# Kernel optimization log

Measured on AMD Instinct MI355X. Metric: run time of the kernel, lower is better.

Reference implementation:

```python
import jax, jax.numpy as jnp
import numpy as np
import math

B, S, H, K = 512, 200, 256, 16

def setup_inputs() -> dict:
    key = jax.random.key(0)
    ks = jax.random.split(key, 8)
    scale = 1.0 / math.sqrt(H)
    return {
        "input_tensor": jax.random.normal(ks[0], (B, S, H), dtype=jnp.float32),
        "item_mask": jax.random.randint(ks[1], (B, S, 1), 0, 2) > 0,
        "time_f_w_matrix": jax.random.uniform(ks[2], (B, S, 1), dtype=jnp.float32),
        "W1": jax.random.normal(ks[3], (H, H), dtype=jnp.float32) * scale,
        "b1": jnp.zeros((H,), dtype=jnp.float32),
        "W2": jax.random.normal(ks[4], (H, H), dtype=jnp.float32) * scale,
        "b2": jnp.zeros((H,), dtype=jnp.float32),
        "W3": jax.random.normal(ks[5], (H, K), dtype=jnp.float32) * scale,
    }

def reference(input_tensor, item_mask, time_f_w_matrix, W1, b1, W2, b2, W3):
    # small MLP: two Linear+ReLU then bias-free Linear to k_interests
    h = jax.nn.relu(jnp.einsum('bsh,hd->bsd', input_tensor, W1) + b1)
    h = jax.nn.relu(jnp.einsum('bsh,hd->bsd', h, W2) + b2)
    D = jnp.einsum('bsh,hk->bsk', h, W3)              # [B,S,K]
    D = jax.nn.softmax(D, axis=-1)                    # softmax over interests
    mask = item_mask[:, :, 0:1]                       # [B,S,1] bool, broadcast over K
    D = jnp.where(mask, D, jnp.float32(-10000.0))
    D = D / jnp.float32(math.sqrt(K))
    D = jax.nn.softmax(D, axis=-2)                    # softmax over sequence
    D = time_f_w_matrix[:, :, 0:1] * D                # time weighting
    # einsum 'nij,nik->nkj': pool items into K interest vectors
    return jnp.einsum('bsh,bsk->bkh', input_tensor, D)
```

## Files before the change

kernel.cpp:

```cpp
#include <hip/hip_runtime.h>
#include <math.h>

#define HDIM 256
#define KDIM 16
#define SDIM 200
#define BDIM 512
#define NROWS (BDIM * SDIM)
#define TM 32

typedef __bf16 bf16x8 __attribute__((ext_vector_type(8)));
typedef __bf16 bf16x4 __attribute__((ext_vector_type(4)));
typedef float  f32x4  __attribute__((ext_vector_type(4)));

__global__ __launch_bounds__(256) void pack_all(
    const float* __restrict__ W1, const float* __restrict__ W2,
    const float* __restrict__ W3,
    __bf16* __restrict__ w1h, __bf16* __restrict__ w1l,
    __bf16* __restrict__ w2h, __bf16* __restrict__ w2l,
    __bf16* __restrict__ w3h, __bf16* __restrict__ w3l)
{
    int gid = blockIdx.x * 256 + threadIdx.x;
    const float* src;
    __bf16 *oh, *ol;
    int e, N;
    if (gid < 65536)       { src = W1; oh = w1h; ol = w1l; e = gid;          N = 256; }
    else if (gid < 131072) { src = W2; oh = w2h; ol = w2l; e = gid - 65536;  N = 256; }
    else if (gid < 135168) { src = W3; oh = w3h; ol = w3l; e = gid - 131072; N = 16;  }
    else return;

    int j  = e & 7;
    int n  = (e >> 3) & (N - 1);
    int kg = e >> 3; kg = (N == 256) ? (kg >> 8) : (kg >> 4);
    int k  = kg * 8 + j;
    float v = src[k * N + n];
    __bf16 h = (__bf16)v;
    oh[e] = h;
    ol[e] = (__bf16)(v - (float)h);
}

__global__ __launch_bounds__(256) void mlp_softk_mfma(
    const float* __restrict__ X, const int* __restrict__ mask,
    const __bf16* __restrict__ W1h, const __bf16* __restrict__ W1l,
    const float* __restrict__ b1,
    const __bf16* __restrict__ W2h, const __bf16* __restrict__ W2l,
    const float* __restrict__ b2,
    const __bf16* __restrict__ W3h, const __bf16* __restrict__ W3l,
    float* __restrict__ P)
{
    __shared__ __bf16 Ahi[TM * HDIM];
    __shared__ __bf16 Alo[TM * HDIM];

    const int tid  = threadIdx.x;
    const int lane = tid & 63;
    const int w    = tid >> 6;
    const int l15  = lane & 15;
    const int quad = lane >> 4;
    const long r0  = (long)blockIdx.x * TM;

    {
        const float4* Xt = (const float4*)(X + r0 * HDIM);
        #pragma unroll
        for (int t = 0; t < (TM * HDIM / 4) / 256; ++t) {
            int v4  = tid + t * 256;
            float4 f = Xt[v4];
            int row = v4 >> 6;
            int col = (v4 & 63) << 2;
            int kgs = (col >> 3) ^ (row & 31);
            int base = row * HDIM + kgs * 8 + (col & 7);
            __bf16 h0 = (__bf16)f.x, h1 = (__bf16)f.y,
                   h2 = (__bf16)f.z, h3 = (__bf16)f.w;
            bf16x4 hv = {h0, h1, h2, h3};
            bf16x4 lv = {(__bf16)(f.x - (float)h0), (__bf16)(f.y - (float)h1),
                         (__bf16)(f.z - (float)h2), (__bf16)(f.w - (float)h3)};
            *(bf16x4*)(&Ahi[base]) = hv;
            *(bf16x4*)(&Alo[base]) = lv;
        }
    }
    __syncthreads();

    f32x4 acc[2][4];

    auto layer = [&](const __bf16* __restrict__ Wh, const __bf16* __restrict__ Wl,
                     const float* __restrict__ bias) {
        #pragma unroll
        for (int mt = 0; mt < 2; ++mt)
            #pragma unroll
            for (int nt = 0; nt < 4; ++nt)
                acc[mt][nt] = (f32x4){0.f, 0.f, 0.f, 0.f};

        #pragma unroll
        for (int kc = 0; kc < 8; ++kc) {
            bf16x8 bh[4], bl[4], ah[2], al[2];
            #pragma unroll
            for (int nt = 0; nt < 4; ++nt) {
                int n  = w * 64 + nt * 16 + l15;
                int kg = kc * 4 + quad;
                bh[nt] = *(const bf16x8*)(Wh + (kg * HDIM + n) * 8);
                bl[nt] = *(const bf16x8*)(Wl + (kg * HDIM + n) * 8);
            }
            #pragma unroll
            for (int mt = 0; mt < 2; ++mt) {
                int row = mt * 16 + l15;
                int kgs = (kc * 4 + quad) ^ (row & 31);
                ah[mt] = *(const bf16x8*)(&Ahi[row * HDIM + kgs * 8]);
                al[mt] = *(const bf16x8*)(&Alo[row * HDIM + kgs * 8]);
            }
            #pragma unroll
            for (int mt = 0; mt < 2; ++mt)
                #pragma unroll
                for (int nt = 0; nt < 4; ++nt) {
                    acc[mt][nt] = __builtin_amdgcn_mfma_f32_16x16x32_bf16(
                        ah[mt], bh[nt], acc[mt][nt], 0, 0, 0);
                    acc[mt][nt] = __builtin_amdgcn_mfma_f32_16x16x32_bf16(
                        al[mt], bh[nt], acc[mt][nt], 0, 0, 0);
                    acc[mt][nt] = __builtin_amdgcn_mfma_f32_16x16x32_bf16(
                        ah[mt], bl[nt], acc[mt][nt], 0, 0, 0);
                }
        }
        __syncthreads();

        float bias_v[4];
        #pragma unroll
        for (int nt = 0; nt < 4; ++nt) bias_v[nt] = bias[w * 64 + nt * 16 + l15];
        #pragma unroll
        for (int mt = 0; mt < 2; ++mt)
            #pragma unroll
            for (int nt = 0; nt < 4; ++nt)
                #pragma unroll
                for (int r = 0; r < 4; ++r) {
                    float v = fmaxf(acc[mt][nt][r] + bias_v[nt], 0.f);
                    int row = mt * 16 + quad * 4 + r;
                    int col = w * 64 + nt * 16 + l15;
                    int idx = row * HDIM + (((col >> 3) ^ (row & 31)) * 8) + (col & 7);
                    __bf16 h = (__bf16)v;
                    Ahi[idx] = h;
                    Alo[idx] = (__bf16)(v - (float)h);
                }
        __syncthreads();
    };

    layer(W1h, W1l, b1);
    layer(W2h, W2l, b2);

    if (w < 2) {
        f32x4 lg = {0.f, 0.f, 0.f, 0.f};
        #pragma unroll
        for (int kc = 0; kc < 8; ++kc) {
            int row = w * 16 + l15;
            int kg  = kc * 4 + quad;
            int kgs = kg ^ (row & 31);
            bf16x8 ah = *(const bf16x8*)(&Ahi[row * HDIM + kgs * 8]);
            bf16x8 al = *(const bf16x8*)(&Alo[row * HDIM + kgs * 8]);
            bf16x8 bh = *(const bf16x8*)(W3h + (kg * KDIM + l15) * 8);
            bf16x8 bl = *(const bf16x8*)(W3l + (kg * KDIM + l15) * 8);
            lg = __builtin_amdgcn_mfma_f32_16x16x32_bf16(ah, bh, lg, 0, 0, 0);
            lg = __builtin_amdgcn_mfma_f32_16x16x32_bf16(al, bh, lg, 0, 0, 0);
            lg = __builtin_amdgcn_mfma_f32_16x16x32_bf16(ah, bl, lg, 0, 0, 0);
        }

        #pragma unroll
        for (int r = 0; r < 4; ++r) {
            float v  = lg[r];
            float mx = v;
            mx = fmaxf(mx, __shfl_xor(mx, 1));
            mx = fmaxf(mx, __shfl_xor(mx, 2));
            mx = fmaxf(mx, __shfl_xor(mx, 4));
            mx = fmaxf(mx, __shfl_xor(mx, 8));
            float e = __expf(v - mx);
            float s = e;
            s += __shfl_xor(s, 1);
            s += __shfl_xor(s, 2);
            s += __shfl_xor(s, 4);
            s += __shfl_xor(s, 8);
            int grow = (int)r0 + w * 16 + quad * 4 + r;
            int mv   = mask[grow];
            float ov = mv ? (e / s) * 0.25f : -2500.0f;
            P[(long)grow * KDIM + l15] = ov;
        }
    }
}

__global__ __launch_bounds__(256) void softs_agg_kernel(
    const float* __restrict__ X, const float* __restrict__ tf,
    const float* __restrict__ P, float* __restrict__ out)
{
    __shared__ float wl[SDIM * KDIM];
    __shared__ float tfl[SDIM];
    __shared__ float psum[256];
    __shared__ float invk[KDIM];
    __shared__ float red[KDIM * HDIM];

    const int tid = threadIdx.x;
    const int b   = blockIdx.x;

    const float* Pb = P + (long)b * SDIM * KDIM;
    float ps = 0.f;
    #pragma unroll
    for (int t = 0; t < 13; ++t) {
        int i = tid + t * 256;
        if (i < SDIM * KDIM) {
            float e = __expf(Pb[i]);
            wl[i] = e;
            ps += e;
        }
    }
    psum[tid] = ps;
    if (tid < SDIM) tfl[tid] = tf[b * SDIM + tid];
    __syncthreads();

    if (tid < KDIM) {
        float s = 0.f;
        #pragma unroll
        for (int g = 0; g < 16; ++g) s += psum[tid + g * 16];
        invk[tid] = 1.f / s;
    }
    __syncthreads();

    #pragma unroll
    for (int t = 0; t < 13; ++t) {
        int i = tid + t * 256;
        if (i < SDIM * KDIM) wl[i] *= tfl[i >> 4] * invk[i & 15];
    }
    __syncthreads();

    const int wv = tid >> 6;
    const int sh = wv >> 1;
    const int hh = wv & 1;
    const int ln = tid & 63;

    float accx[KDIM], accy[KDIM];
    #pragma unroll
    for (int k = 0; k < KDIM; ++k) { accx[k] = 0.f; accy[k] = 0.f; }

    const float2* Xb  = (const float2*)(X + (long)b * SDIM * HDIM) + hh * 64 + ln;
    const f32x4*  wl4 = (const f32x4*)wl;
    const int s0 = sh * 100;
    #pragma unroll 4
    for (int si = 0; si < 100; ++si) {
        int s = s0 + si;
        float2 x = Xb[(long)s * (HDIM / 2)];
        f32x4 d0 = wl4[s * 4 + 0];
        f32x4 d1 = wl4[s * 4 + 1];
        f32x4 d2 = wl4[s * 4 + 2];
        f32x4 d3 = wl4[s * 4 + 3];
        #pragma unroll
        for (int j = 0; j < 4; ++j) {
            accx[0 + j]  = fmaf(x.x, d0[j], accx[0 + j]);
            accx[4 + j]  = fmaf(x.x, d1[j], accx[4 + j]);
            accx[8 + j]  = fmaf(x.x, d2[j], accx[8 + j]);
            accx[12 + j] = fmaf(x.x, d3[j], accx[12 + j]);
            accy[0 + j]  = fmaf(x.y, d0[j], accy[0 + j]);
            accy[4 + j]  = fmaf(x.y, d1[j], accy[4 + j]);
            accy[8 + j]  = fmaf(x.y, d2[j], accy[8 + j]);
            accy[12 + j] = fmaf(x.y, d3[j], accy[12 + j]);
        }
    }

    if (sh == 1) {
        #pragma unroll
        for (int k = 0; k < KDIM; ++k) {
            red[k * HDIM + hh * 128 + 2 * ln + 0] = accx[k];
            red[k * HDIM + hh * 128 + 2 * ln + 1] = accy[k];
        }
    }
    __syncthreads();
    if (sh == 0) {
        float* ob = out + (long)b * KDIM * HDIM + hh * 128 + 2 * ln;
        #pragma unroll
        for (int k = 0; k < KDIM; ++k) {
            float2 o;
            o.x = accx[k] + red[k * HDIM + hh * 128 + 2 * ln + 0];
            o.y = accy[k] + red[k * HDIM + hh * 128 + 2 * ln + 1];
            *(float2*)(ob + (long)k * HDIM) = o;
        }
    }
}

extern "C" void kernel_launch(void* const* d_in, const int* in_sizes, int n_in,
                              void* d_out, int out_size, void* d_ws, size_t ws_size,
                              hipStream_t stream) {
    (void)in_sizes; (void)n_in; (void)out_size; (void)ws_size;
    const float* X    = (const float*)d_in[0];
    const int*   mask = (const int*)  d_in[1];
    const float* tf   = (const float*)d_in[2];
    const float* W1   = (const float*)d_in[3];
    const float* b1   = (const float*)d_in[4];
    const float* W2   = (const float*)d_in[5];
    const float* b2   = (const float*)d_in[6];
    const float* W3   = (const float*)d_in[7];
    float* out = (float*)d_out;

    char* ws = (char*)d_ws;
    float*  P   = (float*)ws;
    __bf16* w1h = (__bf16*)(ws + 6553600);
    __bf16* w1l = w1h + 65536;
    __bf16* w2h = w1l + 65536;
    __bf16* w2l = w2h + 65536;
    __bf16* w3h = w2l + 65536;
    __bf16* w3l = w3h + 4096;

    pack_all<<<528, 256, 0, stream>>>(W1, W2, W3, w1h, w1l, w2h, w2l, w3h, w3l);
    mlp_softk_mfma<<<NROWS / TM, 256, 0, stream>>>(X, mask, w1h, w1l, b1,
                                                   w2h, w2l, b2, w3h, w3l, P);
    softs_agg_kernel<<<BDIM, 256, 0, stream>>>(X, tf, P, out);
}
```

Baseline: 263.6 us.

## Widen softs_agg to 512 threads, split K and sequence across waves

```diff
diff --git a/kernel.cpp b/kernel.cpp
--- a/kernel.cpp
+++ b/kernel.cpp
@@ -180,15 +180,15 @@
     }
 }
 
-__global__ __launch_bounds__(256) void softs_agg_kernel(
+__global__ __launch_bounds__(512) void softs_agg_kernel(
     const float* __restrict__ X, const float* __restrict__ tf,
     const float* __restrict__ P, float* __restrict__ out)
 {
     __shared__ float wl[SDIM * KDIM];
     __shared__ float tfl[SDIM];
-    __shared__ float psum[256];
     __shared__ float invk[KDIM];
-    __shared__ float red[KDIM * HDIM];
+    __shared__ float red[6 * 8 * HDIM];
+    float* psum = red;
 
     const int tid = threadIdx.x;
     const int b   = blockIdx.x;
@@ -196,8 +196,8 @@
     const float* Pb = P + (long)b * SDIM * KDIM;
     float ps = 0.f;
     #pragma unroll
-    for (int t = 0; t < 13; ++t) {
-        int i = tid + t * 256;
+    for (int t = 0; t < 7; ++t) {
+        int i = tid + t * 512;
         if (i < SDIM * KDIM) {
             float e = __expf(Pb[i]);
             wl[i] = e;
@@ -211,68 +211,62 @@
     if (tid < KDIM) {
         float s = 0.f;
         #pragma unroll
-        for (int g = 0; g < 16; ++g) s += psum[tid + g * 16];
+        for (int g = 0; g < 32; ++g) s += psum[tid + g * 16];
         invk[tid] = 1.f / s;
     }
     __syncthreads();
 
     #pragma unroll
-    for (int t = 0; t < 13; ++t) {
-        int i = tid + t * 256;
+    for (int t = 0; t < 7; ++t) {
+        int i = tid + t * 512;
         if (i < SDIM * KDIM) wl[i] *= tfl[i >> 4] * invk[i & 15];
     }
     __syncthreads();
 
     const int wv = tid >> 6;
-    const int sh = wv >> 1;
-    const int hh = wv & 1;
+    const int sq = wv >> 1;
+    const int kh = wv & 1;
     const int ln = tid & 63;
 
-    float accx[KDIM], accy[KDIM];
+    f32x4 acc[8];
     #pragma unroll
-    for (int k = 0; k < KDIM; ++k) { accx[k] = 0.f; accy[k] = 0.f; }
-
-    const float2* Xb  = (const float2*)(X + (long)b * SDIM * HDIM) + hh * 64 + ln;
-    const f32x4*  wl4 = (const f32x4*)wl;
-    const int s0 = sh * 100;
-    #pragma unroll 4
-    for (int si = 0; si < 100; ++si) {
+    for (int j = 0; j < 8; ++j) acc[j] = (f32x4){0.f, 0.f, 0.f, 0.f};
+
+    const f32x4* Xb4 = (const f32x4*)(X + (long)b * SDIM * HDIM);
+    const f32x4* wl4 = (const f32x4*)wl;
+    const int s0 = sq * 50;
+    #pragma unroll 5
+    for (int si = 0; si < 50; ++si) {
         int s = s0 + si;
-        float2 x = Xb[(long)s * (HDIM / 2)];
-        f32x4 d0 = wl4[s * 4 + 0];
-        f32x4 d1 = wl4[s * 4 + 1];
-        f32x4 d2 = wl4[s * 4 + 2];
-        f32x4 d3 = wl4[s * 4 + 3];
+        f32x4 x  = Xb4[s * 64 + ln];
+        f32x4 d0 = wl4[s * 4 + 2 * kh + 0];
+        f32x4 d1 = wl4[s * 4 + 2 * kh + 1];
         #pragma unroll
         for (int j = 0; j < 4; ++j) {
-            accx[0 + j]  = fmaf(x.x, d0[j], accx[0 + j]);
-            accx[4 + j]  = fmaf(x.x, d1[j], accx[4 + j]);
-            accx[8 + j]  = fmaf(x.x, d2[j], accx[8 + j]);
-            accx[12 + j] = fmaf(x.x, d3[j], accx[12 + j]);
-            accy[0 + j]  = fmaf(x.y, d0[j], accy[0 + j]);
-            accy[4 + j]  = fmaf(x.y, d1[j], accy[4 + j]);
-            accy[8 + j]  = fmaf(x.y, d2[j], accy[8 + j]);
-            accy[12 + j] = fmaf(x.y, d3[j], accy[12 + j]);
-        }
-    }
-
-    if (sh == 1) {
-        #pragma unroll
-        for (int k = 0; k < KDIM; ++k) {
-            red[k * HDIM + hh * 128 + 2 * ln + 0] = accx[k];
-            red[k * HDIM + hh * 128 + 2 * ln + 1] = accy[k];
-        }
-    }
-    __syncthreads();
-    if (sh == 0) {
-        float* ob = out + (long)b * KDIM * HDIM + hh * 128 + 2 * ln;
-        #pragma unroll
-        for (int k = 0; k < KDIM; ++k) {
-            float2 o;
-            o.x = accx[k] + red[k * HDIM + hh * 128 + 2 * ln + 0];
-            o.y = accy[k] + red[k * HDIM + hh * 128 + 2 * ln + 1];
-            *(float2*)(ob + (long)k * HDIM) = o;
-        }
+            acc[j]     += x * d0[j];
+            acc[4 + j] += x * d1[j];
+        }
+    }
+
+    if (sq > 0) {
+        float* rp = red + (((sq - 1) * 2 + kh) * 8) * HDIM;
+        #pragma unroll
+        for (int j = 0; j < 8; ++j)
+            *(f32x4*)(rp + j * HDIM + 4 * ln) = acc[j];
+    }
+    __syncthreads();
+    if (sq == 0) {
+        #pragma unroll
+        for (int p = 0; p < 3; ++p) {
+            const float* rp = red + ((p * 2 + kh) * 8) * HDIM;
+            #pragma unroll
+            for (int j = 0; j < 8; ++j)
+                acc[j] += *(const f32x4*)(rp + j * HDIM + 4 * ln);
+        }
+        float* ob = out + (long)b * KDIM * HDIM + kh * 8 * HDIM;
+        #pragma unroll
+        for (int j = 0; j < 8; ++j)
+            *(f32x4*)(ob + j * HDIM + 4 * ln) = acc[j];
     }
 }
 
@@ -302,5 +296,5 @@
     pack_all<<<528, 256, 0, stream>>>(W1, W2, W3, w1h, w1l, w2h, w2l, w3h, w3l);
     mlp_softk_mfma<<<NROWS / TM, 256, 0, stream>>>(X, mask, w1h, w1l, b1,
                                                    w2h, w2l, b2, w3h, w3l, P);
-    softs_agg_kernel<<<BDIM, 256, 0, stream>>>(X, tf, P, out);
+    softs_agg_kernel<<<BDIM, 512, 0, stream>>>(X, tf, P, out);
 }
```

New measurement: 260.5 us. Within noise of the previous version (-1.2%).
